# Optimization experiments

Hardware: AMD Instinct MI355X
Metric: run time of the kernel (lower is better)

The kernel has to match this reference:

```python
import jax, jax.numpy as jnp
import numpy as np

HID = 256   # hidden_dim
P = 16      # pool_size
EPS = 1e-5


def _ln(x, g, b):
    m = x.mean(-1, keepdims=True)
    v = x.var(-1, keepdims=True)
    return (x - m) * jax.lax.rsqrt(v + EPS) * g + b


def setup_inputs() -> dict:
    key = jax.random.key(0)
    ks = jax.random.split(key, 12)
    B, Cf, H, W = 8, 512, 64, 64
    Cg = Cf // 2
    Co = Cf // 2
    s = 0.02
    d = {}
    d['e_f'] = jax.random.normal(ks[0], (B, Cf, H, W), jnp.float32)
    d['e_g'] = jax.random.normal(ks[1], (B, Cg, H, W), jnp.float32)
    d['l_feat'] = jax.random.normal(ks[2], (B, 768, 20), jnp.float32)
    d['l_mask'] = jnp.ones((B, 20, 1), jnp.float32)
    d['ln_f_g'] = jnp.ones((Cf,), jnp.float32)
    d['ln_f_b'] = jnp.zeros((Cf,), jnp.float32)
    d['ln_g_g'] = jnp.ones((Cg,), jnp.float32)
    d['ln_g_b'] = jnp.zeros((Cg,), jnp.float32)
    d['wq'] = jax.random.normal(ks[3], (Cf, HID), jnp.float32) * s
    d['bq'] = jnp.zeros((HID,), jnp.float32)
    d['wk'] = jax.random.normal(ks[4], (Cg, HID), jnp.float32) * s
    d['bk'] = jnp.zeros((HID,), jnp.float32)
    d['wv'] = jax.random.normal(ks[5], (Cg, HID), jnp.float32) * s
    d['bv'] = jnp.zeros((HID,), jnp.float32)
    d['wo'] = jax.random.normal(ks[6], (HID, HID), jnp.float32) * s
    d['bo'] = jnp.zeros((HID,), jnp.float32)
    d['dw_k'] = jax.random.normal(ks[7], (HID, 1, 3, 3), jnp.float32) * s  # depthwise kernel (OIHW, I=1)
    d['efp_w'] = jax.random.normal(ks[8], (HID, Cf), jnp.float32) * s     # 1x1 conv v_channels->hidden
    d['efp_b'] = jnp.zeros((HID,), jnp.float32)
    d['outc_w'] = jax.random.normal(ks[9], (Co, HID), jnp.float32) * s    # 1x1 conv hidden->out
    d['outc_b'] = jnp.zeros((Co,), jnp.float32)
    d['bn_g'] = jnp.ones((Co,), jnp.float32)
    d['bn_b'] = jnp.zeros((Co,), jnp.float32)
    d['bn_m'] = jnp.zeros((Co,), jnp.float32)
    d['bn_v'] = jnp.ones((Co,), jnp.float32)
    return d


def reference(e_f, e_g, l_feat, l_mask, ln_f_g, ln_f_b, ln_g_g, ln_g_b,
              wq, bq, wk, bk, wv, bv, wo, bo, dw_k, efp_w, efp_b,
              outc_w, outc_b, bn_g, bn_b, bn_m, bn_v):
    B, Cf, H, W = e_f.shape
    # Q = w_qi(LN(e_f))                                  (B, HW, HID)
    q = _ln(e_f.transpose(0, 2, 3, 1), ln_f_g, ln_f_b).reshape(B, H * W, Cf) @ wq + bq
    # K/V projections from LN(e_g)
    g = _ln(e_g.transpose(0, 2, 3, 1), ln_g_g, ln_g_b).reshape(B, H * W, -1)
    k = (g @ wk + bk).reshape(B, H, W, HID)
    v = (g @ wv + bv).reshape(B, H, W, HID)
    # 16x16 max/avg pooling -> (B, Hp*Wp, HID)
    k = jnp.max(k.reshape(B, H // P, P, W // P, P, HID), axis=(2, 4)).reshape(B, -1, HID)
    v = jnp.mean(v.reshape(B, H // P, P, W // P, P, HID), axis=(2, 4)).reshape(B, -1, HID)
    # pooled attention
    attn = jax.nn.softmax(jnp.einsum('bqd,bkd->bqk', q, k) * (HID ** -0.5), axis=-1)
    a_i = jnp.einsum('bqk,bkd->bqd', attn, v)  # (B, HW, HID)
    # depthwise 3x3 conv on Q (NCHW)
    q_nchw = q.reshape(B, H, W, HID).transpose(0, 3, 1, 2)
    dw = jax.lax.conv_general_dilated(q_nchw, dw_k, (1, 1), [(1, 1), (1, 1)],
                                      feature_group_count=HID)
    combined = dw + a_i.reshape(B, H, W, HID).transpose(0, 3, 1, 2)
    comb = combined.transpose(0, 2, 3, 1).reshape(B, H * W, HID) @ wo + bo
    comb = comb.reshape(B, H, W, HID).transpose(0, 3, 1, 2)
    # 1x1 proj of e_f, elementwise gate
    efp = jnp.einsum('bchw,oc->bohw', e_f, efp_w) + efp_b[None, :, None, None]
    e_a = efp * comb
    # out: 1x1 conv + BN (inference) + ReLU (dropout inactive in eval)
    out = jnp.einsum('bchw,oc->bohw', e_a, outc_w) + outc_b[None, :, None, None]
    scale = (bn_g * jax.lax.rsqrt(bn_v + EPS))[None, :, None, None]
    out = (out - bn_m[None, :, None, None]) * scale + bn_b[None, :, None, None]
    return jax.nn.relu(out)
```

## Files before the change

kernel.cpp:

```cpp
#include <hip/hip_runtime.h>
#include <math.h>

#define EPS 1e-5f

typedef __attribute__((ext_vector_type(8))) short bf16x8;
typedef __attribute__((ext_vector_type(4))) float f32x4;

__device__ __forceinline__ unsigned short f2bf(float f) {
    unsigned int u = __float_as_uint(f);
    u += 0x7fff + ((u >> 16) & 1);
    return (unsigned short)(u >> 16);
}
__device__ __forceinline__ float bf2f(unsigned short h) {
    return __uint_as_float(((unsigned int)h) << 16);
}
__device__ __forceinline__ float lof(unsigned int u) {
    return __uint_as_float(u << 16);
}
__device__ __forceinline__ float hif(unsigned int u) {
    return __uint_as_float(u & 0xffff0000u);
}
__device__ __forceinline__ void async16(void* lds, const void* g) {
    __builtin_amdgcn_global_load_lds(
        (const __attribute__((address_space(1))) unsigned int*)g,
        (__attribute__((address_space(3))) unsigned int*)lds, 16, 0, 0);
}

__global__ __launch_bounds__(256) void prep_all(
    const float* __restrict__ lnfg, const float* __restrict__ lnfb,
    const float* __restrict__ wq, const float* __restrict__ bq,
    const float* __restrict__ efpw, const float* __restrict__ efpb,
    const float* __restrict__ lngg, const float* __restrict__ lngb,
    const float* __restrict__ wk, const float* __restrict__ bk,
    const float* __restrict__ wv, const float* __restrict__ bv,
    const float* __restrict__ wo, const float* __restrict__ outcw,
    const float* __restrict__ outcb, const float* __restrict__ bng,
    const float* __restrict__ bnb, const float* __restrict__ bnm,
    const float* __restrict__ bnv, const float* __restrict__ dwk,
    unsigned short* __restrict__ Wb1t, unsigned short* __restrict__ Wb2t,
    unsigned short* __restrict__ Wot, unsigned short* __restrict__ Woc,
    float* __restrict__ dwt,
    float* __restrict__ cs1, float* __restrict__ cst1,
    float* __restrict__ cs2, float* __restrict__ cst2,
    float* __restrict__ scv, float* __restrict__ shv)
{
    int idx = blockIdx.x * 256 + threadIdx.x;
    if (idx < 262144) {
        int n = idx >> 9, k = idx & 511;
        float v = (n < 256) ? lnfg[k] * wq[k * 256 + n]
                            : efpw[(size_t)(n - 256) * 512 + k];
        Wb1t[idx] = f2bf(v);
    } else if (idx < 327680) {
        int j = idx - 262144; int n = j >> 8, k = j & 255;
        Wb2t[j] = f2bf(lngg[k] * wk[k * 256 + n]);
    } else if (idx < 393216) {
        int j = idx - 327680; int n = j >> 8, k = j & 255;
        Wot[j] = f2bf(wo[k * 256 + n]);
    } else if (idx < 458752) {
        int j = idx - 393216;
        Woc[j] = f2bf(outcw[j]);
    } else if (idx < 461056) {
        int j = idx - 458752; int tap = j >> 8, ch = j & 255;
        dwt[j] = dwk[ch * 9 + tap];
    } else if (idx < 462336) {
        int j = idx - 461056;
        if (j < 256) {
            int n = j; float cs = 0.f, ct = 0.f;
            for (int k = 0; k < 512; k++) {
                float w = wq[k * 256 + n];
                cs += lnfg[k] * w; ct += lnfb[k] * w;
            }
            cs1[n] = cs; cst1[n] = ct + bq[n];
        } else if (j < 512) {
            cs1[j] = 0.f; cst1[j] = efpb[j - 256];
        } else if (j < 768) {
            int n = j - 512; float cs = 0.f, ct = 0.f;
            for (int k = 0; k < 256; k++) {
                float w = wk[k * 256 + n];
                cs += lngg[k] * w; ct += lngb[k] * w;
            }
            cs2[n] = cs; cst2[n] = ct + bk[n];
        } else if (j < 1024) {
            int n = j - 768; float cs = 0.f, ct = 0.f;
            for (int k = 0; k < 256; k++) {
                float w = wv[k * 256 + n];
                cs += lngg[k] * w; ct += lngb[k] * w;
            }
            cs2[256 + n] = cs; cst2[256 + n] = ct + bv[n];
        } else {
            int n = j - 1024;
            float s = bng[n] * rsqrtf(bnv[n] + EPS);
            scv[n] = s;
            shv[n] = (outcb[n] - bnm[n]) * s + bnb[n];
        }
    }
}

__global__ __launch_bounds__(256) void transpose_fg(
    const float* __restrict__ ef, const float* __restrict__ eg,
    unsigned short* __restrict__ ef_bf, unsigned short* __restrict__ eg_bf,
    float* __restrict__ pf, float* __restrict__ pfq,
    float* __restrict__ pg, float* __restrict__ pgq)
{
    __shared__ float tile[64][65];
    __shared__ float psum[4][64], pss[4][64];
    int id = blockIdx.x;
    const float* src; unsigned short* dst; float* ps; float* pq;
    int C, cblk, b, p0;
    if (id < 4096) {
        src = ef; dst = ef_bf; ps = pf; pq = pfq; C = 512;
        p0 = (id & 63) * 64; cblk = (id >> 6) & 7; b = id >> 9;
    } else {
        id -= 4096;
        src = eg; dst = eg_bf; ps = pg; pq = pgq; C = 256;
        p0 = (id & 63) * 64; cblk = (id >> 6) & 3; b = id >> 8;
    }
    int c0 = cblk * 64;
    const float* s = src + ((size_t)b * C + c0) * 4096 + p0;
    int t = threadIdx.x;
    int lane = t & 63, grp = t >> 6;
#pragma unroll
    for (int i = 0; i < 16; i++) {
        int c = i * 4 + grp;
        tile[c][lane] = s[(size_t)c * 4096 + lane];
    }
    __syncthreads();
    unsigned short* d = dst + ((size_t)(b * 4096 + p0)) * C + c0;
#pragma unroll
    for (int i = 0; i < 16; i++) {
        int p = i * 4 + grp;
        d[(size_t)p * C + lane] = f2bf(tile[lane][p]);
    }
    float sm = 0.f, sq = 0.f;
#pragma unroll
    for (int j = 0; j < 16; j++) {
        float v = tile[grp * 16 + j][lane];
        sm += v; sq += v * v;
    }
    psum[grp][lane] = sm; pss[grp][lane] = sq;
    __syncthreads();
    if (t < 64) {
        float fs = psum[0][t] + psum[1][t] + psum[2][t] + psum[3][t];
        float fq = pss[0][t] + pss[1][t] + pss[2][t] + pss[3][t];
        ps[cblk * 32768 + b * 4096 + p0 + t] = fs;
        pq[cblk * 32768 + b * 4096 + p0 + t] = fq;
    }
}

__global__ __launch_bounds__(256) void ln_finalize(
    const float* __restrict__ pf, const float* __restrict__ pfq,
    const float* __restrict__ pg, const float* __restrict__ pgq,
    float* __restrict__ mf, float* __restrict__ rf,
    float* __restrict__ mg, float* __restrict__ rg)
{
    int gp = blockIdx.x * 256 + threadIdx.x;
    float s = 0.f, q = 0.f;
#pragma unroll
    for (int i = 0; i < 8; i++) { s += pf[i * 32768 + gp]; q += pfq[i * 32768 + gp]; }
    float m = s * (1.f / 512.f);
    float v = q * (1.f / 512.f) - m * m;
    mf[gp] = m; rf[gp] = rsqrtf(v + EPS);
    s = 0.f; q = 0.f;
#pragma unroll
    for (int i = 0; i < 4; i++) { s += pg[i * 32768 + gp]; q += pgq[i * 32768 + gp]; }
    m = s * (1.f / 256.f);
    v = q * (1.f / 256.f) - m * m;
    mg[gp] = m; rg[gp] = rsqrtf(v + EPS);
}

template<int K>
__device__ __forceinline__ void mfma_core(
    const unsigned short* __restrict__ A, const unsigned short* __restrict__ Bt,
    int m0, int n0, unsigned short* As, unsigned short* Bs, f32x4 acc[4][4])
{
    const int tid = threadIdx.x;
    const int wave = tid >> 6, lane = tid & 63;
    const int wm = (wave & 1) * 64, wn = (wave >> 1) * 64;
#pragma unroll
    for (int i = 0; i < 4; i++)
#pragma unroll
        for (int j = 0; j < 4; j++) acc[i][j] = (f32x4){0.f, 0.f, 0.f, 0.f};

    const int srow = wave * 32 + (lane >> 3);
    const int sg = (lane & 7) ^ ((lane >> 3) & 7);
    const unsigned short* ga = A + (size_t)(m0 + srow) * K + sg * 8;
    const unsigned short* gb = Bt + (size_t)(n0 + srow) * K + sg * 8;

    for (int k0 = 0; k0 < K; k0 += 64) {
#pragma unroll
        for (int t = 0; t < 4; t++) {
            async16(As + (wave * 32 + t * 8) * 64, ga + (size_t)t * 8 * K + k0);
            async16(Bs + (wave * 32 + t * 8) * 64, gb + (size_t)t * 8 * K + k0);
        }
        __syncthreads();
#pragma unroll
        for (int ks = 0; ks < 2; ks++) {
            bf16x8 af[4], bfr[4];
            int kb = ks * 4 + (lane >> 4);
            int slot = (kb ^ (lane & 7)) * 8;
#pragma unroll
            for (int i = 0; i < 4; i++) {
                int m = wm + i * 16 + (lane & 15);
                af[i] = *(const bf16x8*)&As[m * 64 + slot];
                int n = wn + i * 16 + (lane & 15);
                bfr[i] = *(const bf16x8*)&Bs[n * 64 + slot];
            }
#pragma unroll
            for (int i = 0; i < 4; i++)
#pragma unroll
                for (int j = 0; j < 4; j++)
                    acc[i][j] = __builtin_amdgcn_mfma_f32_16x16x32_bf16(
                        af[i], bfr[j], acc[i][j], 0, 0, 0);
        }
        __syncthreads();
    }
}

__global__ __launch_bounds__(256) void gemm1_mfma(
    const unsigned short* __restrict__ ef_bf, const unsigned short* __restrict__ Wb1t,
    const float* __restrict__ cs1, const float* __restrict__ cst1,
    const float* __restrict__ mf, const float* __restrict__ rf,
    unsigned short* __restrict__ qbuf, unsigned short* __restrict__ efpbuf)
{
    __shared__ unsigned short As[8192], Bs[8192];
    f32x4 acc[4][4];
    int m0 = blockIdx.x * 128, n0 = blockIdx.y * 128;
    mfma_core<512>(ef_bf, Wb1t, m0, n0, As, Bs, acc);
    int lane = threadIdx.x & 63, wave = threadIdx.x >> 6;
    int wm = (wave & 1) * 64, wn = (wave >> 1) * 64;
    bool isq = (n0 < 256);
#pragma unroll
    for (int i = 0; i < 4; i++) {
#pragma unroll
        for (int r = 0; r < 4; r++) {
            int gm = m0 + wm + i * 16 + ((lane >> 4) * 4) + r;
            float mean = mf[gm], rs = rf[gm];
#pragma unroll
            for (int j = 0; j < 4; j++) {
                int n = n0 + wn + j * 16 + (lane & 15);
                float v = acc[i][j][r];
                if (isq) {
                    float o = rs * (v - mean * cs1[n]) + cst1[n];
                    qbuf[(size_t)gm * 256 + n] = f2bf(o);
                } else {
                    efpbuf[(size_t)gm * 256 + (n - 256)] = f2bf(v + cst1[n]);
                }
            }
        }
    }
}

__global__ __launch_bounds__(256) void gemm2k_mfma(
    const unsigned short* __restrict__ eg_bf, const unsigned short* __restrict__ Wb2t,
    const float* __restrict__ cs2, const float* __restrict__ cst2,
    const float* __restrict__ mg, const float* __restrict__ rg,
    unsigned short* __restrict__ kfull)
{
    __shared__ unsigned short As[8192], Bs[8192];
    f32x4 acc[4][4];
    int m0 = blockIdx.x * 128, n0 = blockIdx.y * 128;
    mfma_core<256>(eg_bf, Wb2t, m0, n0, As, Bs, acc);
    int lane = threadIdx.x & 63, wave = threadIdx.x >> 6;
    int wm = (wave & 1) * 64, wn = (wave >> 1) * 64;
#pragma unroll
    for (int i = 0; i < 4; i++) {
#pragma unroll
        for (int r = 0; r < 4; r++) {
            int gm = m0 + wm + i * 16 + ((lane >> 4) * 4) + r;
            float mean = mg[gm], rs = rg[gm];
#pragma unroll
            for (int j = 0; j < 4; j++) {
                int n = n0 + wn + j * 16 + (lane & 15);
                float o = rs * (acc[i][j][r] - mean * cs2[n]) + cst2[n];
                kfull[(size_t)gm * 256 + n] = f2bf(o);
            }
        }
    }
}

__global__ __launch_bounds__(256) void gemm3_mfma(
    const unsigned short* __restrict__ comb, const unsigned short* __restrict__ Wot,
    const float* __restrict__ bo, const unsigned short* __restrict__ efp,
    unsigned short* __restrict__ ea)
{
    __shared__ unsigned short As[8192], Bs[8192];
    f32x4 acc[4][4];
    int m0 = blockIdx.x * 128, n0 = blockIdx.y * 128;
    mfma_core<256>(comb, Wot, m0, n0, As, Bs, acc);
    int lane = threadIdx.x & 63, wave = threadIdx.x >> 6;
    int wm = (wave & 1) * 64, wn = (wave >> 1) * 64;
#pragma unroll
    for (int i = 0; i < 4; i++) {
#pragma unroll
        for (int r = 0; r < 4; r++) {
            int gm = m0 + wm + i * 16 + ((lane >> 4) * 4) + r;
#pragma unroll
            for (int j = 0; j < 4; j++) {
                int n = n0 + wn + j * 16 + (lane & 15);
                float o = (acc[i][j][r] + bo[n]) * bf2f(efp[(size_t)gm * 256 + n]);
                ea[(size_t)gm * 256 + n] = f2bf(o);
            }
        }
    }
}

__global__ __launch_bounds__(256) void gemm4_mfma(
    const unsigned short* __restrict__ Woc, const unsigned short* __restrict__ ea,
    const float* __restrict__ scv, const float* __restrict__ shv,
    float* __restrict__ outp)
{
    __shared__ unsigned short As[8192], Bs[8192];
    f32x4 acc[4][4];
    int m0 = blockIdx.x * 128, n0 = blockIdx.y * 128;
    mfma_core<256>(Woc, ea, m0, n0, As, Bs, acc);
    int lane = threadIdx.x & 63, wave = threadIdx.x >> 6;
    int wm = (wave & 1) * 64, wn = (wave >> 1) * 64;
#pragma unroll
    for (int i = 0; i < 4; i++) {
#pragma unroll
        for (int r = 0; r < 4; r++) {
            int co = m0 + wm + i * 16 + ((lane >> 4) * 4) + r;
            float s = scv[co], hh = shv[co];
#pragma unroll
            for (int j = 0; j < 4; j++) {
                int p = n0 + wn + j * 16 + (lane & 15);
                float o = fmaxf(fmaf(acc[i][j][r], s, hh), 0.f);
                outp[((size_t)(p >> 12)) * 1048576 + (size_t)co * 4096 + (p & 4095)] = o;
            }
        }
    }
}

__global__ __launch_bounds__(256) void pool_phase(
    const unsigned short* __restrict__ kfull, const float* __restrict__ eg,
    const float* __restrict__ rg, const float* __restrict__ mg,
    unsigned short* __restrict__ kpb, float* __restrict__ s1,
    float* __restrict__ s0)
{
    __shared__ float smem[4352];
    int id = blockIdx.x;
    int t = threadIdx.x;
    if (id < 128) {
        int b = id >> 4, cell = id & 15;
        int hp = cell >> 2, wp = cell & 3;
        int g8 = t & 31, rr = t >> 5;
        float kmx[8];
#pragma unroll
        for (int j = 0; j < 8; j++) kmx[j] = -3.402823466e38f;
#pragma unroll
        for (int rsub = 0; rsub < 2; rsub++) {
            int r = rr * 2 + rsub;
            int prow = (hp * 16 + r) * 64 + wp * 16;
            for (int cl = 0; cl < 16; cl++) {
                size_t basei = ((size_t)(b * 4096 + prow + cl)) * 256 + g8 * 8;
                uint4 kv = *(const uint4*)(kfull + basei);
                kmx[0] = fmaxf(kmx[0], lof(kv.x)); kmx[1] = fmaxf(kmx[1], hif(kv.x));
                kmx[2] = fmaxf(kmx[2], lof(kv.y)); kmx[3] = fmaxf(kmx[3], hif(kv.y));
                kmx[4] = fmaxf(kmx[4], lof(kv.z)); kmx[5] = fmaxf(kmx[5], hif(kv.z));
                kmx[6] = fmaxf(kmx[6], lof(kv.w)); kmx[7] = fmaxf(kmx[7], hif(kv.w));
            }
        }
#pragma unroll
        for (int j = 0; j < 8; j++) smem[rr * 256 + g8 * 8 + j] = kmx[j];
        __syncthreads();
        float m = smem[t];
#pragma unroll
        for (int r2 = 1; r2 < 8; r2++) m = fmaxf(m, smem[r2 * 256 + t]);
        kpb[(size_t)(b * 16 + cell) * 256 + t] = f2bf(m);
    } else {
        int id2 = id - 128;
        int b = id2 >> 6, hp = (id2 >> 4) & 3, cgrp = id2 & 15;
        int rr = t >> 4, cq = t & 15, cx = cq >> 2;
        int p = (hp * 16 + rr) * 64 + cq * 4;
        float4 w4 = *(const float4*)&rg[b * 4096 + p];
        float part[16];
        const float* egb = eg + ((size_t)b * 256 + cgrp * 16) * 4096 + p;
#pragma unroll
        for (int cc = 0; cc < 16; cc++) {
            float4 v4 = *(const float4*)(egb + (size_t)cc * 4096);
            part[cc] = w4.x * v4.x + w4.y * v4.y + w4.z * v4.z + w4.w * v4.w;
        }
#pragma unroll
        for (int cc = 0; cc < 16; cc++) smem[t * 16 + cc] = part[cc];
        if (cgrp == 0) {
            float4 m4 = *(const float4*)&mg[b * 4096 + p];
            smem[4096 + t] = w4.x * m4.x + w4.y * m4.y + w4.z * m4.z + w4.w * m4.w;
        }
        __syncthreads();
        if (t < 64) {
            int cx2 = t >> 4, cc = t & 15;
            float sacc = 0.f;
#pragma unroll
            for (int rr2 = 0; rr2 < 16; rr2++)
#pragma unroll
                for (int dq = 0; dq < 4; dq++)
                    sacc += smem[(rr2 * 16 + cx2 * 4 + dq) * 16 + cc];
            s1[((size_t)(b * 16 + hp * 4 + cx2)) * 256 + cgrp * 16 + cc] = sacc;
        }
        if (cgrp == 0 && t < 4) {
            float sacc = 0.f;
#pragma unroll
            for (int rr2 = 0; rr2 < 16; rr2++)
#pragma unroll
                for (int dq = 0; dq < 4; dq++)
                    sacc += smem[4096 + rr2 * 16 + t * 4 + dq];
            s0[b * 16 + hp * 4 + t] = sacc;
        }
    }
}

__global__ __launch_bounds__(256) void vpool_gemm(
    const float* __restrict__ s1, const float* __restrict__ s0,
    const float* __restrict__ lngg, const float* __restrict__ wv,
    const float* __restrict__ cs2, const float* __restrict__ cst2,
    float* __restrict__ vp)
{
    int cell = blockIdx.x;
    int n = threadIdx.x;
    const float* s1r = s1 + (size_t)cell * 256;
    float acc = 0.f;
    for (int c = 0; c < 256; c++)
        acc = fmaf(lngg[c] * s1r[c], wv[c * 256 + n], acc);
    vp[(size_t)cell * 256 + n] = acc * (1.f / 256.f)
        - (s0[cell] * (1.f / 256.f)) * cs2[256 + n] + cst2[256 + n];
}

__global__ __launch_bounds__(256) void combined_dw(
    const unsigned short* __restrict__ qbuf, const unsigned short* __restrict__ kpb,
    const float* __restrict__ vp, const float* __restrict__ dwt,
    unsigned short* __restrict__ combined)
{
    __shared__ float attns[256];
    int wave = threadIdx.x >> 6, lane = threadIdx.x & 63;
    int id = blockIdx.x;
    int b = id & 7, seg = id >> 3;
    int pidx0 = seg * 16;

    if (wave == 0) {
        int fr = lane & 15, quad = lane >> 4;
        const unsigned short* qrow = qbuf + (size_t)(b * 4096 + pidx0 + fr) * 256 + quad * 8;
        const unsigned short* krow = kpb + (size_t)(b * 16 + fr) * 256 + quad * 8;
        f32x4 sacc = {0.f, 0.f, 0.f, 0.f};
#pragma unroll
        for (int ks = 0; ks < 8; ks++) {
            bf16x8 af = *(const bf16x8*)(qrow + ks * 32);
            bf16x8 bf_ = *(const bf16x8*)(krow + ks * 32);
            sacc = __builtin_amdgcn_mfma_f32_16x16x32_bf16(af, bf_, sacc, 0, 0, 0);
        }
#pragma unroll
        for (int r = 0; r < 4; r++) {
            float s = sacc[r] * 0.0625f;
            float mx = s;
#pragma unroll
            for (int off = 8; off >= 1; off >>= 1) mx = fmaxf(mx, __shfl_xor(mx, off));
            float e = __expf(s - mx);
            float sum = e;
#pragma unroll
            for (int off = 8; off >= 1; off >>= 1) sum += __shfl_xor(sum, off);
            attns[(quad * 4 + r) * 16 + fr] = e / sum;
        }
    }
    __syncthreads();

    int pidx = pidx0 + wave * 4;
    int h = pidx >> 6, w0 = pidx & 63;
    int o4 = lane * 4;

    float4 kreg[9];
#pragma unroll
    for (int tap = 0; tap < 9; tap++)
        kreg[tap] = *(const float4*)&dwt[tap * 256 + o4];

    float4 acc[4];
#pragma unroll
    for (int i = 0; i < 4; i++) acc[i] = (float4){0.f, 0.f, 0.f, 0.f};

    const float* arow = attns + (wave * 4) * 16;
#pragma unroll
    for (int c = 0; c < 16; c++) {
        float4 v = *(const float4*)&vp[(size_t)(b * 16 + c) * 256 + o4];
#pragma unroll
        for (int i = 0; i < 4; i++) {
            float a = arow[i * 16 + c];
            acc[i].x = fmaf(a, v.x, acc[i].x); acc[i].y = fmaf(a, v.y, acc[i].y);
            acc[i].z = fmaf(a, v.z, acc[i].z); acc[i].w = fmaf(a, v.w, acc[i].w);
        }
    }
#pragma unroll
    for (int dy = 0; dy < 3; dy++) {
        int hh = h + dy - 1;
        if (hh < 0 || hh > 63) continue;
        const unsigned short* qr = qbuf + ((size_t)(b * 4096 + hh * 64)) * 256;
        float4 ft[6];
#pragma unroll
        for (int c = 0; c < 6; c++) {
            int xx = w0 - 1 + c;
            if (xx < 0 || xx > 63) {
                ft[c] = (float4){0.f, 0.f, 0.f, 0.f};
            } else {
                uint2 qa = *(const uint2*)(qr + (size_t)xx * 256 + o4);
                ft[c] = (float4){lof(qa.x), hif(qa.x), lof(qa.y), hif(qa.y)};
            }
        }
#pragma unroll
        for (int dx = 0; dx < 3; dx++) {
            float4 kk = kreg[dy * 3 + dx];
#pragma unroll
            for (int i = 0; i < 4; i++) {
                float4 qv = ft[i + dx];
                acc[i].x = fmaf(qv.x, kk.x, acc[i].x);
                acc[i].y = fmaf(qv.y, kk.y, acc[i].y);
                acc[i].z = fmaf(qv.z, kk.z, acc[i].z);
                acc[i].w = fmaf(qv.w, kk.w, acc[i].w);
            }
        }
    }
#pragma unroll
    for (int i = 0; i < 4; i++) {
        uint2 pk;
        pk.x = (unsigned)f2bf(acc[i].x) | ((unsigned)f2bf(acc[i].y) << 16);
        pk.y = (unsigned)f2bf(acc[i].z) | ((unsigned)f2bf(acc[i].w) << 16);
        *(uint2*)(combined + ((size_t)(b * 4096 + pidx + i)) * 256 + o4) = pk;
    }
}

extern "C" void kernel_launch(void* const* d_in, const int* in_sizes, int n_in,
                              void* d_out, int out_size, void* d_ws, size_t ws_size,
                              hipStream_t stream)
{
    const float* e_f   = (const float*)d_in[0];
    const float* e_g   = (const float*)d_in[1];
    const float* lnfg  = (const float*)d_in[4];
    const float* lnfb  = (const float*)d_in[5];
    const float* lngg  = (const float*)d_in[6];
    const float* lngb  = (const float*)d_in[7];
    const float* wq    = (const float*)d_in[8];
    const float* bq    = (const float*)d_in[9];
    const float* wk    = (const float*)d_in[10];
    const float* bk    = (const float*)d_in[11];
    const float* wv    = (const float*)d_in[12];
    const float* bv    = (const float*)d_in[13];
    const float* wo    = (const float*)d_in[14];
    const float* bo    = (const float*)d_in[15];
    const float* dwk   = (const float*)d_in[16];
    const float* efpw  = (const float*)d_in[17];
    const float* efpb  = (const float*)d_in[18];
    const float* outcw = (const float*)d_in[19];
    const float* outcb = (const float*)d_in[20];
    const float* bng   = (const float*)d_in[21];
    const float* bnb   = (const float*)d_in[22];
    const float* bnm   = (const float*)d_in[23];
    const float* bnv   = (const float*)d_in[24];
    float* outp = (float*)d_out;

    char* base = (char*)d_ws;
    auto alloc = [&](size_t bytes) -> char* {
        char* r = base; base += (bytes + 255) & ~(size_t)255; return r;
    };
    float* pf    = (float*)alloc(8 * 32768 * 4);
    float* pfq   = (float*)alloc(8 * 32768 * 4);
    float* pg    = (float*)alloc(4 * 32768 * 4);
    float* pgq   = (float*)alloc(4 * 32768 * 4);
    float* mf    = (float*)alloc(32768 * 4);
    float* rf    = (float*)alloc(32768 * 4);
    float* mg    = (float*)alloc(32768 * 4);
    float* rg    = (float*)alloc(32768 * 4);
    float* cs1   = (float*)alloc(512 * 4);
    float* cst1  = (float*)alloc(512 * 4);
    float* cs2   = (float*)alloc(512 * 4);
    float* cst2  = (float*)alloc(512 * 4);
    float* scv   = (float*)alloc(256 * 4);
    float* shv   = (float*)alloc(256 * 4);
    float* dwt   = (float*)alloc(9 * 256 * 4);
    unsigned short* Wb1t = (unsigned short*)alloc(262144 * 2);
    unsigned short* Wb2t = (unsigned short*)alloc(65536 * 2);
    unsigned short* Wot  = (unsigned short*)alloc(65536 * 2);
    unsigned short* Woc  = (unsigned short*)alloc(65536 * 2);
    unsigned short* ef_bf = (unsigned short*)alloc((size_t)32768 * 512 * 2);
    unsigned short* eg_bf = (unsigned short*)alloc((size_t)32768 * 256 * 2);
    unsigned short* qbuf  = (unsigned short*)alloc((size_t)32768 * 256 * 2);
    unsigned short* efpbuf = (unsigned short*)alloc((size_t)32768 * 256 * 2);
    unsigned short* kfull = (unsigned short*)alloc((size_t)32768 * 256 * 2);
    unsigned short* ea    = (unsigned short*)alloc((size_t)32768 * 256 * 2);
    unsigned short* kpb  = (unsigned short*)alloc(128 * 256 * 2);
    float* vp    = (float*)alloc(128 * 256 * 4);
    float* s1    = (float*)alloc(128 * 256 * 4);
    float* s0    = (float*)alloc(128 * 4);

    prep_all<<<1806, 256, 0, stream>>>(
        lnfg, lnfb, wq, bq, efpw, efpb, lngg, lngb, wk, bk, wv, bv, wo,
        outcw, outcb, bng, bnb, bnm, bnv, dwk,
        Wb1t, Wb2t, Wot, Woc, dwt, cs1, cst1, cs2, cst2, scv, shv);
    transpose_fg<<<6144, 256, 0, stream>>>(e_f, e_g, ef_bf, eg_bf,
                                           pf, pfq, pg, pgq);
    ln_finalize<<<128, 256, 0, stream>>>(pf, pfq, pg, pgq, mf, rf, mg, rg);
    gemm1_mfma<<<dim3(256, 4), 256, 0, stream>>>(ef_bf, Wb1t, cs1, cst1, mf, rf,
                                                 qbuf, efpbuf);
    gemm2k_mfma<<<dim3(256, 2), 256, 0, stream>>>(eg_bf, Wb2t, cs2, cst2, mg, rg,
                                                  kfull);
    pool_phase<<<640, 256, 0, stream>>>(kfull, e_g, rg, mg, kpb, s1, s0);
    vpool_gemm<<<128, 256, 0, stream>>>(s1, s0, lngg, wv, cs2, cst2, vp);
    combined_dw<<<2048, 256, 0, stream>>>(qbuf, kpb, vp, dwt, kfull);
    gemm3_mfma<<<dim3(256, 2), 256, 0, stream>>>(kfull, Wot, bo,
                                                 efpbuf, ea);
    gemm4_mfma<<<dim3(2, 256), 256, 0, stream>>>(Woc, ea, scv, shv, outp);
}
```

Measured before the change: 332.2 us.

## Fuse output projection and final 1x1 conv GEMMs; vectorize transpose loads/stores

```diff
diff --git a/kernel.cpp b/kernel.cpp
--- a/kernel.cpp
+++ b/kernel.cpp
@@ -118,19 +118,31 @@
     int c0 = cblk * 64;
     const float* s = src + ((size_t)b * C + c0) * 4096 + p0;
     int t = threadIdx.x;
+
+    int cr = t >> 4, p4 = (t & 15) * 4;
+#pragma unroll
+    for (int i = 0; i < 4; i++) {
+        int c = i * 16 + cr;
+        float4 v = *(const float4*)(s + (size_t)c * 4096 + p4);
+        tile[c][p4 + 0] = v.x; tile[c][p4 + 1] = v.y;
+        tile[c][p4 + 2] = v.z; tile[c][p4 + 3] = v.w;
+    }
+    __syncthreads();
+
+    unsigned short* d = dst + ((size_t)(b * 4096 + p0)) * C + c0;
+    int pr = t >> 3, c8 = (t & 7) * 8;
+#pragma unroll
+    for (int i = 0; i < 2; i++) {
+        int p = i * 32 + pr;
+        uint4 pk;
+        pk.x = (unsigned)f2bf(tile[c8 + 0][p]) | ((unsigned)f2bf(tile[c8 + 1][p]) << 16);
+        pk.y = (unsigned)f2bf(tile[c8 + 2][p]) | ((unsigned)f2bf(tile[c8 + 3][p]) << 16);
+        pk.z = (unsigned)f2bf(tile[c8 + 4][p]) | ((unsigned)f2bf(tile[c8 + 5][p]) << 16);
+        pk.w = (unsigned)f2bf(tile[c8 + 6][p]) | ((unsigned)f2bf(tile[c8 + 7][p]) << 16);
+        *(uint4*)(d + (size_t)p * C + c8) = pk;
+    }
+
     int lane = t & 63, grp = t >> 6;
-#pragma unroll
-    for (int i = 0; i < 16; i++) {
-        int c = i * 4 + grp;
-        tile[c][lane] = s[(size_t)c * 4096 + lane];
-    }
-    __syncthreads();
-    unsigned short* d = dst + ((size_t)(b * 4096 + p0)) * C + c0;
-#pragma unroll
-    for (int i = 0; i < 16; i++) {
-        int p = i * 4 + grp;
-        d[(size_t)p * C + lane] = f2bf(tile[lane][p]);
-    }
     float sm = 0.f, sq = 0.f;
 #pragma unroll
     for (int j = 0; j < 16; j++) {
@@ -278,53 +290,123 @@
     }
 }
 
-__global__ __launch_bounds__(256) void gemm3_mfma(
+__global__ __launch_bounds__(256) void gemm34_mfma(
     const unsigned short* __restrict__ comb, const unsigned short* __restrict__ Wot,
     const float* __restrict__ bo, const unsigned short* __restrict__ efp,
-    unsigned short* __restrict__ ea)
-{
-    __shared__ unsigned short As[8192], Bs[8192];
-    f32x4 acc[4][4];
-    int m0 = blockIdx.x * 128, n0 = blockIdx.y * 128;
-    mfma_core<256>(comb, Wot, m0, n0, As, Bs, acc);
-    int lane = threadIdx.x & 63, wave = threadIdx.x >> 6;
-    int wm = (wave & 1) * 64, wn = (wave >> 1) * 64;
-#pragma unroll
-    for (int i = 0; i < 4; i++) {
-#pragma unroll
-        for (int r = 0; r < 4; r++) {
-            int gm = m0 + wm + i * 16 + ((lane >> 4) * 4) + r;
-#pragma unroll
-            for (int j = 0; j < 4; j++) {
-                int n = n0 + wn + j * 16 + (lane & 15);
-                float o = (acc[i][j][r] + bo[n]) * bf2f(efp[(size_t)gm * 256 + n]);
-                ea[(size_t)gm * 256 + n] = f2bf(o);
-            }
-        }
-    }
-}
-
-__global__ __launch_bounds__(256) void gemm4_mfma(
-    const unsigned short* __restrict__ Woc, const unsigned short* __restrict__ ea,
+    const unsigned short* __restrict__ Woc,
     const float* __restrict__ scv, const float* __restrict__ shv,
     float* __restrict__ outp)
 {
-    __shared__ unsigned short As[8192], Bs[8192];
+    __shared__ unsigned short As[64 * 64];
+    __shared__ unsigned short Bs[256 * 64];
+    __shared__ unsigned short eat[64 * 256];
+    const int tid = threadIdx.x;
+    const int wave = tid >> 6, lane = tid & 63;
+    const int m0 = blockIdx.x * 64;
+
+    const int srow = lane >> 3;
+    const int sg = (lane & 7) ^ (srow & 7);
+
     f32x4 acc[4][4];
-    int m0 = blockIdx.x * 128, n0 = blockIdx.y * 128;
-    mfma_core<256>(Woc, ea, m0, n0, As, Bs, acc);
-    int lane = threadIdx.x & 63, wave = threadIdx.x >> 6;
-    int wm = (wave & 1) * 64, wn = (wave >> 1) * 64;
+#pragma unroll
+    for (int i = 0; i < 4; i++)
+#pragma unroll
+        for (int j = 0; j < 4; j++) acc[i][j] = (f32x4){0.f, 0.f, 0.f, 0.f};
+
+    const unsigned short* ga = comb + (size_t)(m0 + wave * 16 + srow) * 256 + sg * 8;
+    const unsigned short* gb = Wot + (size_t)(wave * 64 + srow) * 256 + sg * 8;
+
+    for (int k0 = 0; k0 < 256; k0 += 64) {
+#pragma unroll
+        for (int t = 0; t < 2; t++)
+            async16(As + (wave * 16 + t * 8) * 64, ga + (size_t)t * 8 * 256 + k0);
+#pragma unroll
+        for (int t = 0; t < 8; t++)
+            async16(Bs + (wave * 64 + t * 8) * 64, gb + (size_t)t * 8 * 256 + k0);
+        __syncthreads();
+#pragma unroll
+        for (int ks = 0; ks < 2; ks++) {
+            bf16x8 af[4], bfr[4];
+            int kb = ks * 4 + (lane >> 4);
+            int slot = (kb ^ (lane & 7)) * 8;
+#pragma unroll
+            for (int i = 0; i < 4; i++) {
+                af[i]  = *(const bf16x8*)&As[(i * 16 + (lane & 15)) * 64 + slot];
+                bfr[i] = *(const bf16x8*)&Bs[(wave * 64 + i * 16 + (lane & 15)) * 64 + slot];
+            }
+#pragma unroll
+            for (int i = 0; i < 4; i++)
+#pragma unroll
+                for (int j = 0; j < 4; j++)
+                    acc[i][j] = __builtin_amdgcn_mfma_f32_16x16x32_bf16(
+                        af[i], bfr[j], acc[i][j], 0, 0, 0);
+        }
+        __syncthreads();
+    }
+
+    float bo4[4];
+#pragma unroll
+    for (int j = 0; j < 4; j++) bo4[j] = bo[wave * 64 + j * 16 + (lane & 15)];
 #pragma unroll
     for (int i = 0; i < 4; i++) {
 #pragma unroll
         for (int r = 0; r < 4; r++) {
-            int co = m0 + wm + i * 16 + ((lane >> 4) * 4) + r;
+            int pos = i * 16 + ((lane >> 4) * 4) + r;
+#pragma unroll
+            for (int j = 0; j < 4; j++) {
+                int n = wave * 64 + j * 16 + (lane & 15);
+                float o = (acc[i][j][r] + bo4[j])
+                          * bf2f(efp[(size_t)(m0 + pos) * 256 + n]);
+                int o8 = j * 2 + ((lane >> 3) & 1);
+                int slot = o8 ^ (pos & 7);
+                eat[pos * 256 + wave * 64 + slot * 8 + (lane & 7)] = f2bf(o);
+            }
+        }
+    }
+
+    f32x4 acc2[4][4];
+#pragma unroll
+    for (int i = 0; i < 4; i++)
+#pragma unroll
+        for (int j = 0; j < 4; j++) acc2[i][j] = (f32x4){0.f, 0.f, 0.f, 0.f};
+
+    const unsigned short* gw = Woc + (size_t)(wave * 64 + srow) * 256 + sg * 8;
+    for (int k0 = 0; k0 < 256; k0 += 64) {
+#pragma unroll
+        for (int t = 0; t < 8; t++)
+            async16(Bs + (wave * 64 + t * 8) * 64, gw + (size_t)t * 8 * 256 + k0);
+        __syncthreads();
+        int kc = k0 >> 6;
+#pragma unroll
+        for (int ks = 0; ks < 2; ks++) {
+            bf16x8 af2[4], bf2_[4];
+            int kb = ks * 4 + (lane >> 4);
+            int slot = (kb ^ (lane & 7)) * 8;
+#pragma unroll
+            for (int i = 0; i < 4; i++) {
+                af2[i]  = *(const bf16x8*)&Bs[(wave * 64 + i * 16 + (lane & 15)) * 64 + slot];
+                bf2_[i] = *(const bf16x8*)&eat[(i * 16 + (lane & 15)) * 256 + kc * 64 + slot];
+            }
+#pragma unroll
+            for (int i = 0; i < 4; i++)
+#pragma unroll
+                for (int j = 0; j < 4; j++)
+                    acc2[i][j] = __builtin_amdgcn_mfma_f32_16x16x32_bf16(
+                        af2[i], bf2_[j], acc2[i][j], 0, 0, 0);
+        }
+        __syncthreads();
+    }
+
+#pragma unroll
+    for (int i = 0; i < 4; i++) {
+#pragma unroll
+        for (int r = 0; r < 4; r++) {
+            int co = wave * 64 + i * 16 + ((lane >> 4) * 4) + r;
             float s = scv[co], hh = shv[co];
 #pragma unroll
             for (int j = 0; j < 4; j++) {
-                int p = n0 + wn + j * 16 + (lane & 15);
-                float o = fmaxf(fmaf(acc[i][j][r], s, hh), 0.f);
+                int p = m0 + j * 16 + (lane & 15);
+                float o = fmaxf(fmaf(acc2[i][j][r], s, hh), 0.f);
                 outp[((size_t)(p >> 12)) * 1048576 + (size_t)co * 4096 + (p & 4095)] = o;
             }
         }
@@ -581,7 +663,6 @@
     unsigned short* qbuf  = (unsigned short*)alloc((size_t)32768 * 256 * 2);
     unsigned short* efpbuf = (unsigned short*)alloc((size_t)32768 * 256 * 2);
     unsigned short* kfull = (unsigned short*)alloc((size_t)32768 * 256 * 2);
-    unsigned short* ea    = (unsigned short*)alloc((size_t)32768 * 256 * 2);
     unsigned short* kpb  = (unsigned short*)alloc(128 * 256 * 2);
     float* vp    = (float*)alloc(128 * 256 * 4);
     float* s1    = (float*)alloc(128 * 256 * 4);
@@ -601,7 +682,6 @@
     pool_phase<<<640, 256, 0, stream>>>(kfull, e_g, rg, mg, kpb, s1, s0);
     vpool_gemm<<<128, 256, 0, stream>>>(s1, s0, lngg, wv, cs2, cst2, vp);
     combined_dw<<<2048, 256, 0, stream>>>(qbuf, kpb, vp, dwt, kfull);
-    gemm3_mfma<<<dim3(256, 2), 256, 0, stream>>>(kfull, Wot, bo,
-                                                 efpbuf, ea);
-    gemm4_mfma<<<dim3(2, 256), 256, 0, stream>>>(Woc, ea, scv, shv, outp);
-}
+    gemm34_mfma<<<512, 256, 0, stream>>>(kfull, Wot, bo, efpbuf,
+                                         Woc, scv, shv, outp);
+}
```

New measurement: 323.5 us. 2.6% less time.
